# Optimization experiments

Hardware: AMD Instinct MI355X
Metric: run time of the kernel (lower is better)

The kernel has to match this reference:

```python
import jax, jax.numpy as jnp
import numpy as np

CHANNELS = [4096, 4096, 4096, 4096]
SPARSITY = 0.9  # fraction of weight entries zeroed (sten.random_mask_sparsify frac)
BATCH = 4096


def _sparse_weight(key, out_f, in_f, frac):
    kw, km = jax.random.split(key)
    w = jax.random.normal(kw, (out_f, in_f), dtype=jnp.float32)
    keep = jax.random.uniform(km, (out_f, in_f)) >= frac  # keep ~(1-frac) entries
    return jnp.where(keep, w, 0.0)


def setup_inputs() -> dict:
    key = jax.random.key(0)
    ks = jax.random.split(key, 7)
    x = jax.random.normal(ks[0], (BATCH, CHANNELS[0]), dtype=jnp.float32)
    W1 = _sparse_weight(ks[1], CHANNELS[1], CHANNELS[0], SPARSITY)
    b1 = jax.random.uniform(ks[2], (CHANNELS[1],), dtype=jnp.float32)
    W2 = _sparse_weight(ks[3], CHANNELS[2], CHANNELS[1], SPARSITY)
    b2 = jax.random.uniform(ks[4], (CHANNELS[2],), dtype=jnp.float32)
    W3 = _sparse_weight(ks[5], CHANNELS[3], CHANNELS[2], SPARSITY)
    b3 = jax.random.uniform(ks[6], (CHANNELS[3],), dtype=jnp.float32)
    return {"x": x, "W1": W1, "b1": b1, "W2": W2, "b2": b2, "W3": W3, "b3": b3}


def reference(x, W1, b1, W2, b2, W3, b3):
    # Sequential: Linear -> ReLU -> Linear -> ReLU -> Linear
    # F.linear(x, W, b) == x @ W.T + b; weights already carry the sparsity mask.
    h = x @ W1.T + b1
    h = jax.nn.relu(h)
    h = h @ W2.T + b2
    h = jax.nn.relu(h)
    return h @ W3.T + b3
```

## Files before the change

kernel.cpp:

```cpp
#include <hip/hip_runtime.h>
#include <cstdint>


#define MATN 4096
#define NT (MATN / 64)

typedef _Float16 half8 __attribute__((ext_vector_type(8)));
typedef float f32x4 __attribute__((ext_vector_type(4)));

__device__ __forceinline__ void glds16(const void* g, void* l) {
    __builtin_amdgcn_global_load_lds(
        (const __attribute__((address_space(1))) char*)(uintptr_t)g,
        (__attribute__((address_space(3))) char*)(uintptr_t)l,
        16, 0, 0);
}

__device__ __forceinline__ void cvt_body(const float* __restrict__ in,
                                         _Float16* __restrict__ out, int n8) {
    for (int g = blockIdx.x * 256 + threadIdx.x; g < n8; g += gridDim.x * 256) {
        size_t i = (size_t)g * 8;
        float4 a = *(const float4*)(in + i);
        float4 b = *(const float4*)(in + i + 4);
        half8 o;
        o[0] = (_Float16)a.x; o[1] = (_Float16)a.y;
        o[2] = (_Float16)a.z; o[3] = (_Float16)a.w;
        o[4] = (_Float16)b.x; o[5] = (_Float16)b.y;
        o[6] = (_Float16)b.z; o[7] = (_Float16)b.w;
        *(half8*)(out + i) = o;
    }
}

__global__ __launch_bounds__(256)
void cvt_f16(const float* __restrict__ in, _Float16* __restrict__ out, int n8) {
    cvt_body(in, out, n8);
}

__global__ __launch_bounds__(256)
void cvt_f16_2(const float* __restrict__ i0, _Float16* __restrict__ o0,
               const float* __restrict__ i1, _Float16* __restrict__ o1, int n8) {
    cvt_body(blockIdx.y ? i1 : i0, blockIdx.y ? o1 : o0, n8);
}

__global__ __launch_bounds__(256)
void cvt_f16_4(const float* __restrict__ i0, _Float16* __restrict__ o0,
               const float* __restrict__ i1, _Float16* __restrict__ o1,
               const float* __restrict__ i2, _Float16* __restrict__ o2,
               const float* __restrict__ i3, _Float16* __restrict__ o3, int n8) {
    const float* in;
    _Float16* out;
    switch (blockIdx.y) {
        case 0: in = i0; out = o0; break;
        case 1: in = i1; out = o1; break;
        case 2: in = i2; out = o2; break;
        default: in = i3; out = o3; break;
    }
    cvt_body(in, out, n8);
}

#define MFMA_(d, x, y) d = __builtin_amdgcn_mfma_f32_16x16x32_f16(x, y, d, 0, 0, 0)

template <bool RELU, typename OutT>
__global__ __launch_bounds__(512, 2)
void gemm_bt(const _Float16* __restrict__ A, const _Float16* __restrict__ B,
             const float* __restrict__ bias, OutT* __restrict__ C) {
    __shared__ _Float16 lds[2][4][128 * 64];

    const int tid  = threadIdx.x;
    const int lane = tid & 63;
    const int w    = tid >> 6;
    const int wm   = w >> 2;
    const int wn   = w & 3;
    const int l16  = lane & 15;
    const int kq   = lane >> 4;

    const int bid   = blockIdx.y * 16 + blockIdx.x;
    const int sbid  = (bid & 7) * 32 + (bid >> 3);
    const int tileM = (sbid >> 4) * 256;
    const int tileN = (sbid & 15) * 256;

    const int rin = tid >> 3;
    const int gch = (tid & 7) ^ (rin & 7);
    char* const ldsb = (char*)lds;
    const int wq = w * 1024;

    const _Float16* const arow = A + (size_t)(tileM + rin) * MATN + gch * 8;
    const _Float16* const brow = B + (size_t)(tileN + rin) * MATN + gch * 8;

#define STAGE(Tt, s, rowp, roff)                                               \
    do {                                                                       \
        if ((Tt) < NT) {                                                       \
            const _Float16* g_ = (rowp) + (size_t)(roff) * MATN + (Tt) * 64;   \
            char* l_ = ldsb + ((((Tt) & 1) * 4 + (s)) * 16384) + wq;           \
            glds16(g_, l_);                                                    \
            glds16(g_ + (size_t)64 * MATN, l_ + 8192);                         \
        }                                                                      \
    } while (0)

    const int rbA = (wm * 16 + l16) * 128;
    const int rbB = (wn * 16 + l16) * 128;
    const int ok0 = (kq ^ (l16 & 7)) * 16;
    const int ok1 = ok0 ^ 64;

    half8 a[4][2], b0[2][2], b1[2][2];
    f32x4 acc[8][4] = {};

    STAGE(0, 0, arow, 0);
    STAGE(0, 1, brow, 0);
    STAGE(0, 2, brow, 128);
    STAGE(0, 3, arow, 128);
    STAGE(1, 0, arow, 0);
    STAGE(1, 1, brow, 0);
    STAGE(1, 2, brow, 128);
    asm volatile("s_waitcnt vmcnt(6)" ::: "memory");
    __builtin_amdgcn_s_barrier();

#pragma unroll 2
    for (int T = 0; T < NT; ++T) {
        const char* bufA0 = ldsb + ((T & 1) * 4 + 0) * 16384;
        const char* bufB0 = ldsb + ((T & 1) * 4 + 1) * 16384;
        const char* bufB1 = ldsb + ((T & 1) * 4 + 2) * 16384;
        const char* bufA1 = ldsb + ((T & 1) * 4 + 3) * 16384;

#pragma unroll
        for (int mi = 0; mi < 4; ++mi) {
            a[mi][0] = *(const half8*)(bufA0 + mi * 4096 + rbA + ok0);
            a[mi][1] = *(const half8*)(bufA0 + mi * 4096 + rbA + ok1);
        }
#pragma unroll
        for (int ni = 0; ni < 2; ++ni) {
            b0[ni][0] = *(const half8*)(bufB0 + ni * 8192 + rbB + ok0);
            b0[ni][1] = *(const half8*)(bufB0 + ni * 8192 + rbB + ok1);
        }
        STAGE(T + 1, 3, arow, 128);
        __builtin_amdgcn_s_barrier();
        asm volatile("s_waitcnt lgkmcnt(0)" ::: "memory");
        __builtin_amdgcn_sched_barrier(0);
        __builtin_amdgcn_s_setprio(1);
#pragma unroll
        for (int mi = 0; mi < 4; ++mi)
#pragma unroll
            for (int ni = 0; ni < 2; ++ni) {
                MFMA_(acc[mi][ni], a[mi][0], b0[ni][0]);
                MFMA_(acc[mi][ni], a[mi][1], b0[ni][1]);
            }
        __builtin_amdgcn_s_setprio(0);
        __builtin_amdgcn_s_barrier();

#pragma unroll
        for (int ni = 0; ni < 2; ++ni) {
            b1[ni][0] = *(const half8*)(bufB1 + ni * 8192 + rbB + ok0);
            b1[ni][1] = *(const half8*)(bufB1 + ni * 8192 + rbB + ok1);
        }
        STAGE(T + 2, 0, arow, 0);
        __builtin_amdgcn_s_barrier();
        asm volatile("s_waitcnt lgkmcnt(0)" ::: "memory");
        __builtin_amdgcn_sched_barrier(0);
        __builtin_amdgcn_s_setprio(1);
#pragma unroll
        for (int mi = 0; mi < 4; ++mi)
#pragma unroll
            for (int ni = 0; ni < 2; ++ni) {
                MFMA_(acc[mi][2 + ni], a[mi][0], b1[ni][0]);
                MFMA_(acc[mi][2 + ni], a[mi][1], b1[ni][1]);
            }
        __builtin_amdgcn_s_setprio(0);
        __builtin_amdgcn_s_barrier();

#pragma unroll
        for (int mi = 0; mi < 4; ++mi) {
            a[mi][0] = *(const half8*)(bufA1 + mi * 4096 + rbA + ok0);
            a[mi][1] = *(const half8*)(bufA1 + mi * 4096 + rbA + ok1);
        }
        STAGE(T + 2, 1, brow, 0);
        __builtin_amdgcn_s_barrier();
        asm volatile("s_waitcnt lgkmcnt(0)" ::: "memory");
        __builtin_amdgcn_sched_barrier(0);
        __builtin_amdgcn_s_setprio(1);
#pragma unroll
        for (int mi = 0; mi < 4; ++mi)
#pragma unroll
            for (int ni = 0; ni < 2; ++ni) {
                MFMA_(acc[4 + mi][2 + ni], a[mi][0], b1[ni][0]);
                MFMA_(acc[4 + mi][2 + ni], a[mi][1], b1[ni][1]);
            }
        __builtin_amdgcn_s_setprio(0);
        __builtin_amdgcn_s_barrier();

        STAGE(T + 2, 2, brow, 128);
        __builtin_amdgcn_s_barrier();
        __builtin_amdgcn_s_setprio(1);
#pragma unroll
        for (int mi = 0; mi < 4; ++mi)
#pragma unroll
            for (int ni = 0; ni < 2; ++ni) {
                MFMA_(acc[4 + mi][ni], a[mi][0], b0[ni][0]);
                MFMA_(acc[4 + mi][ni], a[mi][1], b0[ni][1]);
            }
        __builtin_amdgcn_s_setprio(0);
        if (T < NT - 2)
            asm volatile("s_waitcnt vmcnt(6)" ::: "memory");
        else if (T == NT - 2)
            asm volatile("s_waitcnt vmcnt(0)" ::: "memory");
        __builtin_amdgcn_s_barrier();
    }
#undef STAGE

#pragma unroll
    for (int ni = 0; ni < 4; ++ni) {
        const int gn = tileN + ni * 64 + wn * 16 + l16;
        const float bv = bias[gn];
#pragma unroll
        for (int mi = 0; mi < 8; ++mi) {
            const int gm = tileM + mi * 32 + wm * 16 + kq * 4;
#pragma unroll
            for (int r = 0; r < 4; ++r) {
                float v = acc[mi][ni][r] + bv;
                if (RELU) v = v > 0.f ? v : 0.f;
                C[(size_t)(gm + r) * MATN + gn] = (OutT)v;
            }
        }
    }
}

extern "C" void kernel_launch(void* const* d_in, const int* in_sizes, int n_in,
                              void* d_out, int out_size, void* d_ws, size_t ws_size,
                              hipStream_t stream) {
    const float* x  = (const float*)d_in[0];
    const float* W1 = (const float*)d_in[1];
    const float* b1 = (const float*)d_in[2];
    const float* W2 = (const float*)d_in[3];
    const float* b2 = (const float*)d_in[4];
    const float* W3 = (const float*)d_in[5];
    const float* b3 = (const float*)d_in[6];
    float* out = (float*)d_out;

    const size_t MAT = (size_t)MATN * MATN;
    const size_t HB  = MAT * 2;
    const int n8 = (int)(MAT / 8);
    dim3 ggrid(MATN / 256, MATN / 256);

    if (ws_size >= HB * 5) {
        _Float16* xb = (_Float16*)d_ws;
        _Float16* w1 = (_Float16*)((char*)d_ws + HB);
        _Float16* w2 = (_Float16*)((char*)d_ws + HB * 2);
        _Float16* w3 = (_Float16*)((char*)d_ws + HB * 3);
        _Float16* h1 = (_Float16*)((char*)d_ws + HB * 4);
        _Float16* h2 = xb;

        cvt_f16_4<<<dim3(2048, 4), 256, 0, stream>>>(x, xb, W1, w1, W2, w2,
                                                     W3, w3, n8);
        gemm_bt<true, _Float16><<<ggrid, 512, 0, stream>>>(xb, w1, b1, h1);
        gemm_bt<true, _Float16><<<ggrid, 512, 0, stream>>>(h1, w2, b2, h2);
        gemm_bt<false, float><<<ggrid, 512, 0, stream>>>(h2, w3, b3, out);
    } else {
        _Float16* xb = (_Float16*)d_ws;
        _Float16* wb = (_Float16*)((char*)d_ws + HB);
        _Float16* h1 = (_Float16*)((char*)d_ws + HB * 2);
        _Float16* h2 = xb;

        cvt_f16_2<<<dim3(2048, 2), 256, 0, stream>>>(x, xb, W1, wb, n8);
        gemm_bt<true, _Float16><<<ggrid, 512, 0, stream>>>(xb, wb, b1, h1);
        cvt_f16<<<2048, 256, 0, stream>>>(W2, wb, n8);
        gemm_bt<true, _Float16><<<ggrid, 512, 0, stream>>>(h1, wb, b2, h2);
        cvt_f16<<<2048, 256, 0, stream>>>(W3, wb, n8);
        gemm_bt<false, float><<<ggrid, 512, 0, stream>>>(h2, wb, b3, out);
    }
}
```

Baseline: 571.8 us.

## Restructure GEMM main loop into K-half phases with partial LDS waits

The inner loop is reorganized so each of the four MFMA phases consumes one K-half (ok0 or ok1) across all four B column groups, instead of one B group across both K-halves. Global-to-LDS staging is reshuffled: three of the four next-tile buffers are now prefetched only one iteration ahead, and the vmcnt waits are tightened. The lgkmcnt waits become partial so MFMAs can start while later LDS reads are still in flight. This aims to overlap LDS reads with MFMA work and cut stalls, but the shorter global prefetch distance and the new buffer-reuse ordering could expose memory latency or introduce hazards.

```diff
diff --git a/kernel.cpp b/kernel.cpp
--- a/kernel.cpp
+++ b/kernel.cpp
@@ -101,105 +101,98 @@
     const int ok0 = (kq ^ (l16 & 7)) * 16;
     const int ok1 = ok0 ^ 64;
 
-    half8 a[4][2], b0[2][2], b1[2][2];
+    half8 aP[4], aQ[4], bP[4], bQ[4];
     f32x4 acc[8][4] = {};
 
     STAGE(0, 0, arow, 0);
     STAGE(0, 1, brow, 0);
     STAGE(0, 2, brow, 128);
     STAGE(0, 3, arow, 128);
-    STAGE(1, 0, arow, 0);
-    STAGE(1, 1, brow, 0);
     STAGE(1, 2, brow, 128);
-    asm volatile("s_waitcnt vmcnt(6)" ::: "memory");
+    asm volatile("s_waitcnt vmcnt(2)" ::: "memory");
     __builtin_amdgcn_s_barrier();
 
 #pragma unroll 2
     for (int T = 0; T < NT; ++T) {
-        const char* bufA0 = ldsb + ((T & 1) * 4 + 0) * 16384;
-        const char* bufB0 = ldsb + ((T & 1) * 4 + 1) * 16384;
-        const char* bufB1 = ldsb + ((T & 1) * 4 + 2) * 16384;
-        const char* bufA1 = ldsb + ((T & 1) * 4 + 3) * 16384;
-
-#pragma unroll
-        for (int mi = 0; mi < 4; ++mi) {
-            a[mi][0] = *(const half8*)(bufA0 + mi * 4096 + rbA + ok0);
-            a[mi][1] = *(const half8*)(bufA0 + mi * 4096 + rbA + ok1);
-        }
-#pragma unroll
-        for (int ni = 0; ni < 2; ++ni) {
-            b0[ni][0] = *(const half8*)(bufB0 + ni * 8192 + rbB + ok0);
-            b0[ni][1] = *(const half8*)(bufB0 + ni * 8192 + rbB + ok1);
-        }
+        const char* base  = ldsb + (T & 1) * 65536;
+        const char* bufA0 = base;
+        const char* bufB0 = base + 16384;
+        const char* bufB1 = base + 32768;
+        const char* bufA1 = base + 49152;
+
+#pragma unroll
+        for (int mi = 0; mi < 4; ++mi)
+            aP[mi] = *(const half8*)(bufA0 + mi * 4096 + rbA + ok0);
+        bP[0] = *(const half8*)(bufB0 + rbB + ok0);
+        bP[1] = *(const half8*)(bufB0 + 8192 + rbB + ok0);
+        bP[2] = *(const half8*)(bufB1 + rbB + ok0);
+        bP[3] = *(const half8*)(bufB1 + 8192 + rbB + ok0);
+#pragma unroll
+        for (int mi = 0; mi < 4; ++mi)
+            aQ[mi] = *(const half8*)(bufA1 + mi * 4096 + rbA + ok0);
+        STAGE(T + 1, 0, arow, 0);
+        __builtin_amdgcn_s_barrier();
+        asm volatile("s_waitcnt lgkmcnt(4)" ::: "memory");
+        __builtin_amdgcn_sched_barrier(0);
+        __builtin_amdgcn_s_setprio(1);
+#pragma unroll
+        for (int mi = 0; mi < 4; ++mi)
+#pragma unroll
+            for (int ni = 0; ni < 4; ++ni)
+                MFMA_(acc[mi][ni], aP[mi], bP[ni]);
+        __builtin_amdgcn_s_setprio(0);
+        __builtin_amdgcn_s_barrier();
+
+#pragma unroll
+        for (int mi = 0; mi < 4; ++mi)
+            aP[mi] = *(const half8*)(bufA1 + mi * 4096 + rbA + ok1);
+        bQ[0] = *(const half8*)(bufB0 + rbB + ok1);
+        bQ[1] = *(const half8*)(bufB0 + 8192 + rbB + ok1);
+        bQ[2] = *(const half8*)(bufB1 + rbB + ok1);
+        bQ[3] = *(const half8*)(bufB1 + 8192 + rbB + ok1);
         STAGE(T + 1, 3, arow, 128);
         __builtin_amdgcn_s_barrier();
+        asm volatile("s_waitcnt lgkmcnt(8)" ::: "memory");
+        __builtin_amdgcn_sched_barrier(0);
+        __builtin_amdgcn_s_setprio(1);
+#pragma unroll
+        for (int mi = 0; mi < 4; ++mi)
+#pragma unroll
+            for (int ni = 0; ni < 4; ++ni)
+                MFMA_(acc[4 + mi][ni], aQ[mi], bP[ni]);
+        __builtin_amdgcn_s_setprio(0);
+        __builtin_amdgcn_s_barrier();
+
+#pragma unroll
+        for (int mi = 0; mi < 4; ++mi)
+            aQ[mi] = *(const half8*)(bufA0 + mi * 4096 + rbA + ok1);
+        STAGE(T + 1, 1, brow, 0);
+        __builtin_amdgcn_s_barrier();
+        asm volatile("s_waitcnt lgkmcnt(4)" ::: "memory");
+        __builtin_amdgcn_sched_barrier(0);
+        __builtin_amdgcn_s_setprio(1);
+#pragma unroll
+        for (int mi = 0; mi < 4; ++mi)
+#pragma unroll
+            for (int ni = 0; ni < 4; ++ni)
+                MFMA_(acc[4 + mi][ni], aP[mi], bQ[ni]);
+        __builtin_amdgcn_s_setprio(0);
+        __builtin_amdgcn_s_barrier();
+
+        STAGE(T + 2, 2, brow, 128);
+        __builtin_amdgcn_s_barrier();
         asm volatile("s_waitcnt lgkmcnt(0)" ::: "memory");
         __builtin_amdgcn_sched_barrier(0);
         __builtin_amdgcn_s_setprio(1);
 #pragma unroll
         for (int mi = 0; mi < 4; ++mi)
 #pragma unroll
-            for (int ni = 0; ni < 2; ++ni) {
-                MFMA_(acc[mi][ni], a[mi][0], b0[ni][0]);
-                MFMA_(acc[mi][ni], a[mi][1], b0[ni][1]);
-            }
-        __builtin_amdgcn_s_setprio(0);
-        __builtin_amdgcn_s_barrier();
-
-#pragma unroll
-        for (int ni = 0; ni < 2; ++ni) {
-            b1[ni][0] = *(const half8*)(bufB1 + ni * 8192 + rbB + ok0);
-            b1[ni][1] = *(const half8*)(bufB1 + ni * 8192 + rbB + ok1);
-        }
-        STAGE(T + 2, 0, arow, 0);
-        __builtin_amdgcn_s_barrier();
-        asm volatile("s_waitcnt lgkmcnt(0)" ::: "memory");
-        __builtin_amdgcn_sched_barrier(0);
-        __builtin_amdgcn_s_setprio(1);
-#pragma unroll
-        for (int mi = 0; mi < 4; ++mi)
-#pragma unroll
-            for (int ni = 0; ni < 2; ++ni) {
-                MFMA_(acc[mi][2 + ni], a[mi][0], b1[ni][0]);
-                MFMA_(acc[mi][2 + ni], a[mi][1], b1[ni][1]);
-            }
-        __builtin_amdgcn_s_setprio(0);
-        __builtin_amdgcn_s_barrier();
-
-#pragma unroll
-        for (int mi = 0; mi < 4; ++mi) {
-            a[mi][0] = *(const half8*)(bufA1 + mi * 4096 + rbA + ok0);
-            a[mi][1] = *(const half8*)(bufA1 + mi * 4096 + rbA + ok1);
-        }
-        STAGE(T + 2, 1, brow, 0);
-        __builtin_amdgcn_s_barrier();
-        asm volatile("s_waitcnt lgkmcnt(0)" ::: "memory");
-        __builtin_amdgcn_sched_barrier(0);
-        __builtin_amdgcn_s_setprio(1);
-#pragma unroll
-        for (int mi = 0; mi < 4; ++mi)
-#pragma unroll
-            for (int ni = 0; ni < 2; ++ni) {
-                MFMA_(acc[4 + mi][2 + ni], a[mi][0], b1[ni][0]);
-                MFMA_(acc[4 + mi][2 + ni], a[mi][1], b1[ni][1]);
-            }
-        __builtin_amdgcn_s_setprio(0);
-        __builtin_amdgcn_s_barrier();
-
-        STAGE(T + 2, 2, brow, 128);
-        __builtin_amdgcn_s_barrier();
-        __builtin_amdgcn_s_setprio(1);
-#pragma unroll
-        for (int mi = 0; mi < 4; ++mi)
-#pragma unroll
-            for (int ni = 0; ni < 2; ++ni) {
-                MFMA_(acc[4 + mi][ni], a[mi][0], b0[ni][0]);
-                MFMA_(acc[4 + mi][ni], a[mi][1], b0[ni][1]);
-            }
+            for (int ni = 0; ni < 4; ++ni)
+                MFMA_(acc[mi][ni], aQ[mi], bQ[ni]);
         __builtin_amdgcn_s_setprio(0);
         if (T < NT - 2)
-            asm volatile("s_waitcnt vmcnt(6)" ::: "memory");
-        else if (T == NT - 2)
+            asm volatile("s_waitcnt vmcnt(2)" ::: "memory");
+        else
             asm volatile("s_waitcnt vmcnt(0)" ::: "memory");
         __builtin_amdgcn_s_barrier();
     }
```

New measurement: 589.0 us. 3.0% more time.
